# Kernel optimization log

Hardware: AMD Instinct MI355X
Metric: run time of the kernel (lower is better)

The kernel has to match this reference:

```python
import jax, jax.numpy as jnp
import numpy as np

N_NODES = 100000
N_EDGES = 1200000
NODE_DIM = 128
HIDDEN = 64
N_POSTS = 50000


def setup_inputs() -> dict:
    key = jax.random.key(0)
    ks = jax.random.split(key, 10)
    s = 1.0 / np.sqrt(NODE_DIM)
    sh = 1.0 / np.sqrt(HIDDEN)
    return {
        "node_features": jax.random.normal(ks[0], (N_NODES, NODE_DIM), dtype=jnp.float32),
        "edge_index": jax.random.randint(ks[1], (2, N_EDGES), 0, N_NODES, dtype=jnp.int64) if jax.config.jax_enable_x64 else jax.random.randint(ks[1], (2, N_EDGES), 0, N_NODES, dtype=jnp.int32),
        "post_mask": jax.random.randint(ks[2], (N_POSTS,), 0, N_NODES, dtype=jnp.int32),
        "W_enc": jax.random.uniform(ks[3], (NODE_DIM, HIDDEN), jnp.float32, -s, s),
        "b_enc": jax.random.uniform(ks[4], (HIDDEN,), jnp.float32, -s, s),
        "W_conv": jax.random.uniform(ks[5], (HIDDEN, HIDDEN), jnp.float32, -sh, sh),
        "b_conv": jax.random.uniform(ks[6], (HIDDEN,), jnp.float32, -sh, sh),
        "W_out": jax.random.uniform(ks[7], (HIDDEN, 1), jnp.float32, -sh, sh),
        "b_out": jax.random.uniform(ks[8], (1,), jnp.float32, -sh, sh),
    }


def reference(node_features, edge_index, post_mask, W_enc, b_enc, W_conv, b_conv, W_out, b_out):
    # encode: relu(Linear)
    node_emb = jax.nn.relu(node_features @ W_enc + b_enc)  # [N, H]
    src, dst = edge_index[0], edge_index[1]
    # per-edge gather then scatter-add into destination nodes (segment sum)
    messages = jax.ops.segment_sum(node_emb[src], dst, num_segments=node_emb.shape[0])  # [N, H]
    node_emb = jax.nn.relu((node_emb + messages) @ W_conv + b_conv)  # [N, H]
    post_emb = node_emb[post_mask]  # [P, H]
    out = jax.nn.sigmoid((post_emb @ W_out + b_out).squeeze(-1))  # [P]
    return out
```

## Files before the change

kernel.cpp:

```cpp
#include <hip/hip_runtime.h>
#include <hip/hip_bf16.h>
#include <math.h>


#define HIDDEN 64
#define NODE_DIM 128
#define SCAN_CHUNK 1024

typedef __attribute__((ext_vector_type(8))) short short8;
typedef __attribute__((ext_vector_type(4))) float floatx4;

union F2B { short8 s; __hip_bfloat162 h[4]; };

__device__ inline short8 cvt8(const float4& p, const float4& q) {
    F2B u;
    u.h[0] = __float22bfloat162_rn(make_float2(p.x, p.y));
    u.h[1] = __float22bfloat162_rn(make_float2(p.z, p.w));
    u.h[2] = __float22bfloat162_rn(make_float2(q.x, q.y));
    u.h[3] = __float22bfloat162_rn(make_float2(q.z, q.w));
    return u.s;
}

__device__ inline void cvt8_split(const float4& p, const float4& q,
                                  short8& hi, short8& lo) {
    const float f[8] = {p.x, p.y, p.z, p.w, q.x, q.y, q.z, q.w};
    F2B uh, ul;
    #pragma unroll
    for (int jj = 0; jj < 4; ++jj) {
        const float2 v = make_float2(f[2 * jj], f[2 * jj + 1]);
        const __hip_bfloat162 h = __float22bfloat162_rn(v);
        const float2 hv = __bfloat1622float2(h);
        ul.h[jj] = __float22bfloat162_rn(make_float2(v.x - hv.x, v.y - hv.y));
        uh.h[jj] = h;
    }
    hi = uh.s; lo = ul.s;
}

__global__ __launch_bounds__(256) void k_encode_mfma(
    const float* __restrict__ A, const float* __restrict__ We,
    const float* __restrict__ be, __hip_bfloat16* __restrict__ emb16, int n_tiles)
{
    const int lane = threadIdx.x & 63;
    const int r    = lane & 15;
    const int quad = lane >> 4;

    short8 Wb[4][4];
    #pragma unroll
    for (int ks = 0; ks < 4; ++ks) {
        #pragma unroll
        for (int nt = 0; nt < 4; ++nt) {
            F2B u;
            #pragma unroll
            for (int jj = 0; jj < 4; ++jj) {
                const int k0 = ks * 32 + quad * 8 + 2 * jj;
                const float lo = We[(size_t)k0 * HIDDEN + nt * 16 + r];
                const float hi = We[(size_t)(k0 + 1) * HIDDEN + nt * 16 + r];
                u.h[jj] = __float22bfloat162_rn(make_float2(lo, hi));
            }
            Wb[ks][nt] = u.s;
        }
    }
    float bias[4];
    #pragma unroll
    for (int nt = 0; nt < 4; ++nt) bias[nt] = be[nt * 16 + r];

    const int wid    = (blockIdx.x * 256 + threadIdx.x) >> 6;
    const int nwaves = gridDim.x * 4;
    for (int t = wid; t < n_tiles; t += nwaves) {
        const float* Arow = A + (size_t)t * 16 * NODE_DIM + (size_t)r * NODE_DIM + quad * 8;
        float4 a[4][2];
        #pragma unroll
        for (int ks = 0; ks < 4; ++ks) {
            a[ks][0] = *(const float4*)(Arow + ks * 32);
            a[ks][1] = *(const float4*)(Arow + ks * 32 + 4);
        }
        floatx4 acc[4] = {};
        #pragma unroll
        for (int ks = 0; ks < 4; ++ks) {
            const short8 af = cvt8(a[ks][0], a[ks][1]);
            #pragma unroll
            for (int nt = 0; nt < 4; ++nt)
                acc[nt] = __builtin_amdgcn_mfma_f32_16x16x32_bf16(af, Wb[ks][nt], acc[nt], 0, 0, 0);
        }
        #pragma unroll
        for (int nt = 0; nt < 4; ++nt) {
            #pragma unroll
            for (int g = 0; g < 4; ++g) {
                const int node = t * 16 + quad * 4 + g;
                const float h = fmaxf(acc[nt][g] + bias[nt], 0.0f);
                emb16[(size_t)node * HIDDEN + nt * 16 + r] = __float2bfloat16(h);
            }
        }
    }
}

__global__ __launch_bounds__(64) void k_encode_tail(
    const float* __restrict__ A, const float* __restrict__ We,
    const float* __restrict__ be, __hip_bfloat16* __restrict__ emb16, int base)
{
    const int lane = threadIdx.x;
    const int n = base + blockIdx.x;
    const float* row = A + (size_t)n * NODE_DIM;
    float acc = be[lane];
    for (int k = 0; k < NODE_DIM; ++k)
        acc = fmaf(row[k], We[(size_t)k * HIDDEN + lane], acc);
    emb16[(size_t)n * HIDDEN + lane] = __float2bfloat16(fmaxf(acc, 0.0f));
}

__global__ __launch_bounds__(256) void k_setflags(
    const int* __restrict__ post, int* __restrict__ flag,
    unsigned int* __restrict__ bits,
    int* __restrict__ nodelist, int* __restrict__ inv,
    int* __restrict__ listCnt, int n_posts)
{
    const int p = blockIdx.x * 256 + threadIdx.x;
    if (p >= n_posts) return;
    const int n = post[p];
    atomicOr(&bits[n >> 5], 1u << (n & 31));
    if (atomicCAS(&flag[n], 0, 1) == 0) {
        const int i = atomicAdd(listCnt, 1);
        nodelist[i] = n;
        inv[n] = i;
    }
}

__global__ __launch_bounds__(256) void k_count(
    const int* __restrict__ dsts, const unsigned int* __restrict__ bits,
    int* __restrict__ count, int n_edges)
{
    const int stride = gridDim.x * 256;
    for (int e = blockIdx.x * 256 + threadIdx.x; e < n_edges; e += stride) {
        const int d = dsts[e];
        if ((bits[d >> 5] >> (d & 31)) & 1u) atomicAdd(&count[d], 1);
    }
}

__global__ __launch_bounds__(256) void k_scan_lb(
    const int* __restrict__ count, int* __restrict__ row_start,
    unsigned int* __restrict__ partials, int n)
{
    __shared__ int s[256];
    __shared__ int sExc;
    const int b = blockIdx.x, tid = threadIdx.x;
    const int base = b * SCAN_CHUNK + tid * 4;
    int c0 = (base + 0 < n) ? count[base + 0] : 0;
    int c1 = (base + 1 < n) ? count[base + 1] : 0;
    int c2 = (base + 2 < n) ? count[base + 2] : 0;
    int c3 = (base + 3 < n) ? count[base + 3] : 0;
    const int t = c0 + c1 + c2 + c3;
    s[tid] = t;
    __syncthreads();
    #pragma unroll
    for (int off = 1; off < 256; off <<= 1) {
        int v = (tid >= off) ? s[tid - off] : 0;
        __syncthreads();
        s[tid] += v;
        __syncthreads();
    }
    if (tid == 0) {
        const unsigned int total = (unsigned int)s[255];
        if (b == 0) {
            __hip_atomic_store(&partials[0], (2u << 30) | total,
                               __ATOMIC_RELEASE, __HIP_MEMORY_SCOPE_AGENT);
            sExc = 0;
        } else {
            __hip_atomic_store(&partials[b], (1u << 30) | total,
                               __ATOMIC_RELEASE, __HIP_MEMORY_SCOPE_AGENT);
            int exc = 0;
            int j = b - 1;
            while (true) {
                const unsigned int v = __hip_atomic_load(&partials[j],
                    __ATOMIC_ACQUIRE, __HIP_MEMORY_SCOPE_AGENT);
                const unsigned int st = v >> 30;
                if (st == 0u) continue;
                exc += (int)(v & 0x3FFFFFFFu);
                if (st == 2u) break;
                --j;
            }
            __hip_atomic_store(&partials[b], (2u << 30) | (unsigned int)(exc + (int)total),
                               __ATOMIC_RELEASE, __HIP_MEMORY_SCOPE_AGENT);
            sExc = exc;
        }
    }
    __syncthreads();
    int run = sExc + s[tid] - t;
    if (base + 0 < n) row_start[base + 0] = run;           run += c0;
    if (base + 1 < n) row_start[base + 1] = run;           run += c1;
    if (base + 2 < n) row_start[base + 2] = run;           run += c2;
    if (base + 3 < n) row_start[base + 3] = run;
}

__global__ __launch_bounds__(256) void k_fill(
    const int* __restrict__ srcs, const int* __restrict__ dsts,
    const unsigned int* __restrict__ bits, int* __restrict__ row_start,
    int* __restrict__ slots, int n_edges)
{
    const int stride = gridDim.x * 256;
    for (int e = blockIdx.x * 256 + threadIdx.x; e < n_edges; e += stride) {
        const int d = dsts[e];
        if (!((bits[d >> 5] >> (d & 31)) & 1u)) continue;
        const int idx = atomicAdd(&row_start[d], 1);
        slots[idx] = srcs[e];
    }
}

__global__ __launch_bounds__(256) void k_gather(
    const int* __restrict__ nodelist, const int* __restrict__ listCnt,
    const int* __restrict__ row_end, const int* __restrict__ count,
    const int* __restrict__ slots, const __hip_bfloat16* __restrict__ emb16,
    float* __restrict__ msg_c)
{
    const int lane = threadIdx.x & 63;
    const int j    = lane & 7;
    const int g    = lane >> 3;
    const int gw   = (blockIdx.x * 256 + threadIdx.x) >> 6;
    const int nw   = gridDim.x * 4;
    const int nc   = listCnt[0];

    for (int i = gw; i < nc; i += nw) {
        const int n    = nodelist[i];
        const int m    = count[n];
        const int base = row_end[n] - m;

        float2 a0 = {0.f, 0.f}, a1 = {0.f, 0.f}, a2 = {0.f, 0.f}, a3 = {0.f, 0.f};
        #define ACC8(v)  do { F2B u; u.s = (v); float2 t;                       \
            t = __bfloat1622float2(u.h[0]); a0.x += t.x; a0.y += t.y;           \
            t = __bfloat1622float2(u.h[1]); a1.x += t.x; a1.y += t.y;           \
            t = __bfloat1622float2(u.h[2]); a2.x += t.x; a2.y += t.y;           \
            t = __bfloat1622float2(u.h[3]); a3.x += t.x; a3.y += t.y; } while (0)

        if (g == 0) {
            const short8 v = *(const short8*)(emb16 + (size_t)n * HIDDEN + j * 8);
            ACC8(v);
        }
        int c = g;
        for (; c + 8 < m; c += 16) {
            const int s0 = slots[base + c];
            const int s1 = slots[base + c + 8];
            const short8 v0 = *(const short8*)(emb16 + (size_t)s0 * HIDDEN + j * 8);
            const short8 v1 = *(const short8*)(emb16 + (size_t)s1 * HIDDEN + j * 8);
            ACC8(v0); ACC8(v1);
        }
        for (; c < m; c += 8) {
            const int s0 = slots[base + c];
            const short8 v0 = *(const short8*)(emb16 + (size_t)s0 * HIDDEN + j * 8);
            ACC8(v0);
        }
        #undef ACC8

        #pragma unroll
        for (int off = 8; off < 64; off <<= 1) {
            a0.x += __shfl_xor(a0.x, off); a0.y += __shfl_xor(a0.y, off);
            a1.x += __shfl_xor(a1.x, off); a1.y += __shfl_xor(a1.y, off);
            a2.x += __shfl_xor(a2.x, off); a2.y += __shfl_xor(a2.y, off);
            a3.x += __shfl_xor(a3.x, off); a3.y += __shfl_xor(a3.y, off);
        }
        if (g == 0) {
            float4* dst = (float4*)(msg_c + (size_t)i * HIDDEN + j * 8);
            dst[0] = make_float4(a0.x, a0.y, a1.x, a1.y);
            dst[1] = make_float4(a2.x, a2.y, a3.x, a3.y);
        }
    }
}

__global__ __launch_bounds__(256) void k_head_mfma(
    const int* __restrict__ listCnt, const float* __restrict__ msg_c,
    const float* __restrict__ Wc, const float* __restrict__ bc,
    const float* __restrict__ Wo, const float* __restrict__ bo,
    float* __restrict__ res_c)
{
    const int lane = threadIdx.x & 63;
    const int r    = lane & 15;
    const int quad = lane >> 4;

    short8 Wb[2][4];
    #pragma unroll
    for (int ks = 0; ks < 2; ++ks) {
        #pragma unroll
        for (int nt = 0; nt < 4; ++nt) {
            F2B u;
            #pragma unroll
            for (int jj = 0; jj < 4; ++jj) {
                const int k0 = ks * 32 + quad * 8 + 2 * jj;
                const float lo = Wc[(size_t)k0 * HIDDEN + nt * 16 + r];
                const float hi = Wc[(size_t)(k0 + 1) * HIDDEN + nt * 16 + r];
                u.h[jj] = __float22bfloat162_rn(make_float2(lo, hi));
            }
            Wb[ks][nt] = u.s;
        }
    }
    float bias[4], wo[4];
    #pragma unroll
    for (int nt = 0; nt < 4; ++nt) { bias[nt] = bc[nt * 16 + r]; wo[nt] = Wo[nt * 16 + r]; }
    const float bo_s = bo[0];

    const int nc      = listCnt[0];
    const int n_tiles = (nc + 15) / 16;
    const int wid     = (blockIdx.x * 256 + threadIdx.x) >> 6;
    const int nwaves  = gridDim.x * 4;

    for (int tile = wid; tile < n_tiles; tile += nwaves) {
        const int i0  = tile * 16;
        const int row = i0 + r;
        floatx4 acc[4] = {};
        #pragma unroll
        for (int ks = 0; ks < 2; ++ks) {
            float4 f0 = make_float4(0.f, 0.f, 0.f, 0.f), f1 = f0;
            if (row < nc) {
                const float* src = msg_c + (size_t)row * HIDDEN + ks * 32 + quad * 8;
                f0 = *(const float4*)src;
                f1 = *(const float4*)(src + 4);
            }
            short8 ah, al;
            cvt8_split(f0, f1, ah, al);
            #pragma unroll
            for (int nt = 0; nt < 4; ++nt) {
                acc[nt] = __builtin_amdgcn_mfma_f32_16x16x32_bf16(ah, Wb[ks][nt], acc[nt], 0, 0, 0);
                acc[nt] = __builtin_amdgcn_mfma_f32_16x16x32_bf16(al, Wb[ks][nt], acc[nt], 0, 0, 0);
            }
        }
        float res[4];
        #pragma unroll
        for (int gg = 0; gg < 4; ++gg) {
            float part = 0.0f;
            #pragma unroll
            for (int nt = 0; nt < 4; ++nt)
                part += fmaxf(acc[nt][gg] + bias[nt], 0.0f) * wo[nt];
            part += __shfl_xor(part, 1);
            part += __shfl_xor(part, 2);
            part += __shfl_xor(part, 4);
            part += __shfl_xor(part, 8);
            res[gg] = part;
        }
        if (r == 0) {
            #pragma unroll
            for (int gg = 0; gg < 4; ++gg) {
                const int idx = i0 + quad * 4 + gg;
                if (idx < nc)
                    res_c[idx] = 1.0f / (1.0f + __expf(-(res[gg] + bo_s)));
            }
        }
    }
}

__global__ __launch_bounds__(256) void k_out(
    const int* __restrict__ post, const int* __restrict__ inv,
    const float* __restrict__ res_c, float* __restrict__ out, int n_posts)
{
    const int p = blockIdx.x * 256 + threadIdx.x;
    if (p < n_posts) out[p] = res_c[inv[post[p]]];
}

extern "C" void kernel_launch(void* const* d_in, const int* in_sizes, int n_in,
                              void* d_out, int out_size, void* d_ws, size_t ws_size,
                              hipStream_t stream) {
    const float* A    = (const float*)d_in[0];
    const int*   ei   = (const int*)  d_in[1];
    const int*   post = (const int*)  d_in[2];
    const float* We   = (const float*)d_in[3];
    const float* be   = (const float*)d_in[4];
    const float* Wc   = (const float*)d_in[5];
    const float* bc   = (const float*)d_in[6];
    const float* Wo   = (const float*)d_in[7];
    const float* bo   = (const float*)d_in[8];
    float* out = (float*)d_out;

    const int n_nodes = in_sizes[0] / NODE_DIM;
    const int n_edges = in_sizes[1] / 2;
    const int n_posts = in_sizes[2];

    char* p = (char*)d_ws;
    __hip_bfloat16* emb16 = (__hip_bfloat16*)p;  p += (size_t)n_nodes * HIDDEN * 2;
    float* msg_c    = (float*)p;              p += (size_t)n_posts * HIDDEN * 4;
    int*   slots    = (int*)p;                p += (size_t)n_edges * 4;
    int*   flag     = (int*)p;                p += (size_t)n_nodes * 4;
    int*   count    = (int*)p;                p += (size_t)n_nodes * 4;
    int*   listCnt  = (int*)p;                p += 256;
    unsigned int* partials = (unsigned int*)p; p += 512;
    unsigned int* bits = (unsigned int*)p;    p += 16384;
    int*   row_start= (int*)p;                p += (size_t)n_nodes * 4;
    int*   nodelist = (int*)p;                p += (size_t)n_nodes * 4;
    int*   inv      = (int*)p;                p += (size_t)n_nodes * 4;
    float* res_c    = (float*)p;              p += (size_t)n_posts * 4;

    const int* srcs = ei;
    const int* dsts = ei + n_edges;
    const int nb = (n_nodes + SCAN_CHUNK - 1) / SCAN_CHUNK;
    const int n_tiles = n_nodes / 16;
    const int rem     = n_nodes - n_tiles * 16;

    hipMemsetAsync(flag, 0, (size_t)n_nodes * 8 + 256 + 512 + 16384, stream);
    k_setflags<<<(n_posts + 255) / 256, 256, 0, stream>>>(post, flag, bits, nodelist, inv, listCnt, n_posts);
    k_encode_mfma<<<(n_tiles + 3) / 4, 256, 0, stream>>>(A, We, be, emb16, n_tiles);
    if (rem > 0)
        k_encode_tail<<<rem, 64, 0, stream>>>(A, We, be, emb16, n_tiles * 16);
    k_count<<<2048, 256, 0, stream>>>(dsts, bits, count, n_edges);
    k_scan_lb<<<nb, 256, 0, stream>>>(count, row_start, partials, n_nodes);
    k_fill<<<2048, 256, 0, stream>>>(srcs, dsts, bits, row_start, slots, n_edges);
    k_gather<<<8192, 256, 0, stream>>>(nodelist, listCnt, row_start, count, slots, emb16, msg_c);
    k_head_mfma<<<1024, 256, 0, stream>>>(listCnt, msg_c, Wc, bc, Wo, bo, res_c);
    k_out<<<(n_posts + 255) / 256, 256, 0, stream>>>(post, inv, res_c, out, n_posts);
}
```

Measured before the change: 223.4 us.

## Fuse encode and CSR build into one persistent kernel with grid barriers

Merges encode, setflags, count, scan and fill into a single persistent kernel. Blocks are split into an encode group and a CSR-build group that run at the same time, and the build phases are separated by software grid barriers on atomic counters. The aim is to cut five launches and their serial gaps and to overlap the encode matmul with the edge counting and filling. This depends on every build block being co-resident for the spin barriers. The encode now runs on fewer blocks, the scan needs at least 98 build blocks, and the flag array is replaced by the bitset's atomicOr return value.

```diff
diff --git a/kernel.cpp b/kernel.cpp
--- a/kernel.cpp
+++ b/kernel.cpp
@@ -36,171 +36,176 @@
     hi = uh.s; lo = ul.s;
 }
 
-__global__ __launch_bounds__(256) void k_encode_mfma(
-    const float* __restrict__ A, const float* __restrict__ We,
-    const float* __restrict__ be, __hip_bfloat16* __restrict__ emb16, int n_tiles)
+__device__ inline void cbar(int* ctr, int target) {
+    __syncthreads();
+    if (threadIdx.x == 0) {
+        __builtin_amdgcn_fence(__ATOMIC_RELEASE, "agent");
+        __hip_atomic_fetch_add(ctr, 1, __ATOMIC_RELAXED, __HIP_MEMORY_SCOPE_AGENT);
+        while (__hip_atomic_load(ctr, __ATOMIC_RELAXED, __HIP_MEMORY_SCOPE_AGENT) < target)
+            __builtin_amdgcn_s_sleep(8);
+        __builtin_amdgcn_fence(__ATOMIC_ACQUIRE, "agent");
+    }
+    __syncthreads();
+}
+
+struct BuildP {
+    const float* A; const int* srcs; const int* dsts; const int* post;
+    const float* We; const float* be;
+    __hip_bfloat16* emb16;
+    int* slots; int* count; int* listCnt;
+    unsigned int* partials; unsigned int* bits;
+    int* row_start; int* nodelist; int* inv; int* bars;
+    int n_nodes, n_edges, n_posts, n_tiles, eblk, cblk;
+};
+
+__global__ __launch_bounds__(256, 2) void k_build(BuildP P)
 {
-    const int lane = threadIdx.x & 63;
+    const int tid  = threadIdx.x;
+    const int lane = tid & 63;
     const int r    = lane & 15;
     const int quad = lane >> 4;
 
-    short8 Wb[4][4];
-    #pragma unroll
-    for (int ks = 0; ks < 4; ++ks) {
-        #pragma unroll
-        for (int nt = 0; nt < 4; ++nt) {
-            F2B u;
-            #pragma unroll
-            for (int jj = 0; jj < 4; ++jj) {
-                const int k0 = ks * 32 + quad * 8 + 2 * jj;
-                const float lo = We[(size_t)k0 * HIDDEN + nt * 16 + r];
-                const float hi = We[(size_t)(k0 + 1) * HIDDEN + nt * 16 + r];
-                u.h[jj] = __float22bfloat162_rn(make_float2(lo, hi));
-            }
-            Wb[ks][nt] = u.s;
-        }
-    }
-    float bias[4];
-    #pragma unroll
-    for (int nt = 0; nt < 4; ++nt) bias[nt] = be[nt * 16 + r];
-
-    const int wid    = (blockIdx.x * 256 + threadIdx.x) >> 6;
-    const int nwaves = gridDim.x * 4;
-    for (int t = wid; t < n_tiles; t += nwaves) {
-        const float* Arow = A + (size_t)t * 16 * NODE_DIM + (size_t)r * NODE_DIM + quad * 8;
-        float4 a[4][2];
-        #pragma unroll
-        for (int ks = 0; ks < 4; ++ks) {
-            a[ks][0] = *(const float4*)(Arow + ks * 32);
-            a[ks][1] = *(const float4*)(Arow + ks * 32 + 4);
-        }
-        floatx4 acc[4] = {};
-        #pragma unroll
-        for (int ks = 0; ks < 4; ++ks) {
-            const short8 af = cvt8(a[ks][0], a[ks][1]);
+    if ((int)blockIdx.x < P.eblk) {
+        short8 Wb[4][4];
+        #pragma unroll
+        for (int ks = 0; ks < 4; ++ks)
+            #pragma unroll
+            for (int nt = 0; nt < 4; ++nt) {
+                F2B u;
+                #pragma unroll
+                for (int jj = 0; jj < 4; ++jj) {
+                    const int k0 = ks * 32 + quad * 8 + 2 * jj;
+                    const float lo = P.We[(size_t)k0 * HIDDEN + nt * 16 + r];
+                    const float hi = P.We[(size_t)(k0 + 1) * HIDDEN + nt * 16 + r];
+                    u.h[jj] = __float22bfloat162_rn(make_float2(lo, hi));
+                }
+                Wb[ks][nt] = u.s;
+            }
+        float bias[4];
+        #pragma unroll
+        for (int nt = 0; nt < 4; ++nt) bias[nt] = P.be[nt * 16 + r];
+
+        const int widE = blockIdx.x * 4 + (tid >> 6);
+        const int nwE  = P.eblk * 4;
+        for (int t = widE; t < P.n_tiles; t += nwE) {
+            const float* Arow = P.A + (size_t)t * 16 * NODE_DIM + (size_t)r * NODE_DIM + quad * 8;
+            float4 a[4][2];
+            #pragma unroll
+            for (int ks = 0; ks < 4; ++ks) {
+                a[ks][0] = *(const float4*)(Arow + ks * 32);
+                a[ks][1] = *(const float4*)(Arow + ks * 32 + 4);
+            }
+            floatx4 acc[4] = {};
+            #pragma unroll
+            for (int ks = 0; ks < 4; ++ks) {
+                const short8 af = cvt8(a[ks][0], a[ks][1]);
+                #pragma unroll
+                for (int nt = 0; nt < 4; ++nt)
+                    acc[nt] = __builtin_amdgcn_mfma_f32_16x16x32_bf16(af, Wb[ks][nt], acc[nt], 0, 0, 0);
+            }
             #pragma unroll
             for (int nt = 0; nt < 4; ++nt)
-                acc[nt] = __builtin_amdgcn_mfma_f32_16x16x32_bf16(af, Wb[ks][nt], acc[nt], 0, 0, 0);
-        }
-        #pragma unroll
-        for (int nt = 0; nt < 4; ++nt) {
-            #pragma unroll
-            for (int g = 0; g < 4; ++g) {
-                const int node = t * 16 + quad * 4 + g;
-                const float h = fmaxf(acc[nt][g] + bias[nt], 0.0f);
-                emb16[(size_t)node * HIDDEN + nt * 16 + r] = __float2bfloat16(h);
-            }
-        }
-    }
-}
-
-__global__ __launch_bounds__(64) void k_encode_tail(
-    const float* __restrict__ A, const float* __restrict__ We,
-    const float* __restrict__ be, __hip_bfloat16* __restrict__ emb16, int base)
-{
-    const int lane = threadIdx.x;
-    const int n = base + blockIdx.x;
-    const float* row = A + (size_t)n * NODE_DIM;
-    float acc = be[lane];
-    for (int k = 0; k < NODE_DIM; ++k)
-        acc = fmaf(row[k], We[(size_t)k * HIDDEN + lane], acc);
-    emb16[(size_t)n * HIDDEN + lane] = __float2bfloat16(fmaxf(acc, 0.0f));
-}
-
-__global__ __launch_bounds__(256) void k_setflags(
-    const int* __restrict__ post, int* __restrict__ flag,
-    unsigned int* __restrict__ bits,
-    int* __restrict__ nodelist, int* __restrict__ inv,
-    int* __restrict__ listCnt, int n_posts)
-{
-    const int p = blockIdx.x * 256 + threadIdx.x;
-    if (p >= n_posts) return;
-    const int n = post[p];
-    atomicOr(&bits[n >> 5], 1u << (n & 31));
-    if (atomicCAS(&flag[n], 0, 1) == 0) {
-        const int i = atomicAdd(listCnt, 1);
-        nodelist[i] = n;
-        inv[n] = i;
-    }
-}
-
-__global__ __launch_bounds__(256) void k_count(
-    const int* __restrict__ dsts, const unsigned int* __restrict__ bits,
-    int* __restrict__ count, int n_edges)
-{
-    const int stride = gridDim.x * 256;
-    for (int e = blockIdx.x * 256 + threadIdx.x; e < n_edges; e += stride) {
-        const int d = dsts[e];
-        if ((bits[d >> 5] >> (d & 31)) & 1u) atomicAdd(&count[d], 1);
-    }
-}
-
-__global__ __launch_bounds__(256) void k_scan_lb(
-    const int* __restrict__ count, int* __restrict__ row_start,
-    unsigned int* __restrict__ partials, int n)
-{
-    __shared__ int s[256];
-    __shared__ int sExc;
-    const int b = blockIdx.x, tid = threadIdx.x;
-    const int base = b * SCAN_CHUNK + tid * 4;
-    int c0 = (base + 0 < n) ? count[base + 0] : 0;
-    int c1 = (base + 1 < n) ? count[base + 1] : 0;
-    int c2 = (base + 2 < n) ? count[base + 2] : 0;
-    int c3 = (base + 3 < n) ? count[base + 3] : 0;
-    const int t = c0 + c1 + c2 + c3;
-    s[tid] = t;
-    __syncthreads();
-    #pragma unroll
-    for (int off = 1; off < 256; off <<= 1) {
-        int v = (tid >= off) ? s[tid - off] : 0;
-        __syncthreads();
-        s[tid] += v;
-        __syncthreads();
-    }
-    if (tid == 0) {
-        const unsigned int total = (unsigned int)s[255];
-        if (b == 0) {
-            __hip_atomic_store(&partials[0], (2u << 30) | total,
-                               __ATOMIC_RELEASE, __HIP_MEMORY_SCOPE_AGENT);
-            sExc = 0;
-        } else {
-            __hip_atomic_store(&partials[b], (1u << 30) | total,
-                               __ATOMIC_RELEASE, __HIP_MEMORY_SCOPE_AGENT);
-            int exc = 0;
-            int j = b - 1;
-            while (true) {
-                const unsigned int v = __hip_atomic_load(&partials[j],
-                    __ATOMIC_ACQUIRE, __HIP_MEMORY_SCOPE_AGENT);
-                const unsigned int st = v >> 30;
-                if (st == 0u) continue;
-                exc += (int)(v & 0x3FFFFFFFu);
-                if (st == 2u) break;
-                --j;
-            }
-            __hip_atomic_store(&partials[b], (2u << 30) | (unsigned int)(exc + (int)total),
-                               __ATOMIC_RELEASE, __HIP_MEMORY_SCOPE_AGENT);
-            sExc = exc;
-        }
-    }
-    __syncthreads();
-    int run = sExc + s[tid] - t;
-    if (base + 0 < n) row_start[base + 0] = run;           run += c0;
-    if (base + 1 < n) row_start[base + 1] = run;           run += c1;
-    if (base + 2 < n) row_start[base + 2] = run;           run += c2;
-    if (base + 3 < n) row_start[base + 3] = run;
-}
-
-__global__ __launch_bounds__(256) void k_fill(
-    const int* __restrict__ srcs, const int* __restrict__ dsts,
-    const unsigned int* __restrict__ bits, int* __restrict__ row_start,
-    int* __restrict__ slots, int n_edges)
-{
-    const int stride = gridDim.x * 256;
-    for (int e = blockIdx.x * 256 + threadIdx.x; e < n_edges; e += stride) {
-        const int d = dsts[e];
-        if (!((bits[d >> 5] >> (d & 31)) & 1u)) continue;
-        const int idx = atomicAdd(&row_start[d], 1);
-        slots[idx] = srcs[e];
+                #pragma unroll
+                for (int g = 0; g < 4; ++g) {
+                    const int node = t * 16 + quad * 4 + g;
+                    const float h = fmaxf(acc[nt][g] + bias[nt], 0.0f);
+                    P.emb16[(size_t)node * HIDDEN + nt * 16 + r] = __float2bfloat16(h);
+                }
+        }
+        const int rem = P.n_nodes - P.n_tiles * 16;
+        if (rem > 0 && widE == 0) {
+            for (int n = P.n_tiles * 16; n < P.n_nodes; ++n) {
+                float acc = P.be[lane];
+                const float* row = P.A + (size_t)n * NODE_DIM;
+                for (int k = 0; k < NODE_DIM; ++k)
+                    acc = fmaf(row[k], P.We[(size_t)k * HIDDEN + lane], acc);
+                P.emb16[(size_t)n * HIDDEN + lane] = __float2bfloat16(fmaxf(acc, 0.0f));
+            }
+        }
+    } else {
+        const int cb    = blockIdx.x - P.eblk;
+        const int ctid  = cb * 256 + tid;
+        const int cstep = P.cblk * 256;
+
+        for (int p = ctid; p < P.n_posts; p += cstep) {
+            const int n = P.post[p];
+            const unsigned int bit = 1u << (n & 31);
+            const unsigned int old = atomicOr(&P.bits[n >> 5], bit);
+            if (!(old & bit)) {
+                const int i = atomicAdd(P.listCnt, 1);
+                P.nodelist[i] = n;
+                P.inv[n] = i;
+            }
+        }
+        cbar(P.bars + 0, P.cblk);
+
+        for (int e = ctid; e < P.n_edges; e += cstep) {
+            const int d = P.dsts[e];
+            if ((P.bits[d >> 5] >> (d & 31)) & 1u) atomicAdd(&P.count[d], 1);
+        }
+        cbar(P.bars + 1, P.cblk);
+
+        {
+            __shared__ int s[256];
+            __shared__ int sExc;
+            const int nb = (P.n_nodes + SCAN_CHUNK - 1) / SCAN_CHUNK;
+            if (cb < nb) {
+                const int base = cb * SCAN_CHUNK + tid * 4;
+                const int n = P.n_nodes;
+                int c0 = (base + 0 < n) ? P.count[base + 0] : 0;
+                int c1 = (base + 1 < n) ? P.count[base + 1] : 0;
+                int c2 = (base + 2 < n) ? P.count[base + 2] : 0;
+                int c3 = (base + 3 < n) ? P.count[base + 3] : 0;
+                const int t4 = c0 + c1 + c2 + c3;
+                s[tid] = t4;
+                __syncthreads();
+                #pragma unroll
+                for (int off = 1; off < 256; off <<= 1) {
+                    int v = (tid >= off) ? s[tid - off] : 0;
+                    __syncthreads();
+                    s[tid] += v;
+                    __syncthreads();
+                }
+                if (tid == 0) {
+                    const unsigned int total = (unsigned int)s[255];
+                    if (cb == 0) {
+                        __hip_atomic_store(&P.partials[0], (2u << 30) | total,
+                                           __ATOMIC_RELEASE, __HIP_MEMORY_SCOPE_AGENT);
+                        sExc = 0;
+                    } else {
+                        __hip_atomic_store(&P.partials[cb], (1u << 30) | total,
+                                           __ATOMIC_RELEASE, __HIP_MEMORY_SCOPE_AGENT);
+                        int exc = 0, j = cb - 1;
+                        while (true) {
+                            const unsigned int v = __hip_atomic_load(&P.partials[j],
+                                __ATOMIC_ACQUIRE, __HIP_MEMORY_SCOPE_AGENT);
+                            const unsigned int st = v >> 30;
+                            if (st == 0u) { __builtin_amdgcn_s_sleep(1); continue; }
+                            exc += (int)(v & 0x3FFFFFFFu);
+                            if (st == 2u) break;
+                            --j;
+                        }
+                        __hip_atomic_store(&P.partials[cb], (2u << 30) | (unsigned int)(exc + (int)total),
+                                           __ATOMIC_RELEASE, __HIP_MEMORY_SCOPE_AGENT);
+                        sExc = exc;
+                    }
+                }
+                __syncthreads();
+                int run = sExc + s[tid] - t4;
+                if (base + 0 < n) P.row_start[base + 0] = run;   run += c0;
+                if (base + 1 < n) P.row_start[base + 1] = run;   run += c1;
+                if (base + 2 < n) P.row_start[base + 2] = run;   run += c2;
+                if (base + 3 < n) P.row_start[base + 3] = run;
+            }
+        }
+        cbar(P.bars + 2, P.cblk);
+
+        for (int e = ctid; e < P.n_edges; e += cstep) {
+            const int d = P.dsts[e];
+            if (!((P.bits[d >> 5] >> (d & 31)) & 1u)) continue;
+            const int idx = atomicAdd(&P.row_start[d], 1);
+            P.slots[idx] = P.srcs[e];
+        }
     }
 }
 
@@ -275,7 +280,7 @@
 
     short8 Wb[2][4];
     #pragma unroll
-    for (int ks = 0; ks < 2; ++ks) {
+    for (int ks = 0; ks < 2; ++ks)
         #pragma unroll
         for (int nt = 0; nt < 4; ++nt) {
             F2B u;
@@ -288,7 +293,6 @@
             }
             Wb[ks][nt] = u.s;
         }
-    }
     float bias[4], wo[4];
     #pragma unroll
     for (int nt = 0; nt < 4; ++nt) { bias[nt] = bc[nt * 16 + r]; wo[nt] = Wo[nt * 16 + r]; }
@@ -354,50 +358,58 @@
 extern "C" void kernel_launch(void* const* d_in, const int* in_sizes, int n_in,
                               void* d_out, int out_size, void* d_ws, size_t ws_size,
                               hipStream_t stream) {
-    const float* A    = (const float*)d_in[0];
-    const int*   ei   = (const int*)  d_in[1];
-    const int*   post = (const int*)  d_in[2];
-    const float* We   = (const float*)d_in[3];
-    const float* be   = (const float*)d_in[4];
-    const float* Wc   = (const float*)d_in[5];
-    const float* bc   = (const float*)d_in[6];
-    const float* Wo   = (const float*)d_in[7];
-    const float* bo   = (const float*)d_in[8];
+    BuildP P;
+    P.A    = (const float*)d_in[0];
+    const int* ei = (const int*)d_in[1];
+    P.post = (const int*)d_in[2];
+    P.We   = (const float*)d_in[3];
+    P.be   = (const float*)d_in[4];
+    const float* Wc = (const float*)d_in[5];
+    const float* bc = (const float*)d_in[6];
+    const float* Wo = (const float*)d_in[7];
+    const float* bo = (const float*)d_in[8];
     float* out = (float*)d_out;
 
-    const int n_nodes = in_sizes[0] / NODE_DIM;
-    const int n_edges = in_sizes[1] / 2;
-    const int n_posts = in_sizes[2];
+    P.n_nodes = in_sizes[0] / NODE_DIM;
+    P.n_edges = in_sizes[1] / 2;
+    P.n_posts = in_sizes[2];
+    P.n_tiles = P.n_nodes / 16;
+    P.srcs = ei;
+    P.dsts = ei + P.n_edges;
 
     char* p = (char*)d_ws;
-    __hip_bfloat16* emb16 = (__hip_bfloat16*)p;  p += (size_t)n_nodes * HIDDEN * 2;
-    float* msg_c    = (float*)p;              p += (size_t)n_posts * HIDDEN * 4;
-    int*   slots    = (int*)p;                p += (size_t)n_edges * 4;
-    int*   flag     = (int*)p;                p += (size_t)n_nodes * 4;
-    int*   count    = (int*)p;                p += (size_t)n_nodes * 4;
-    int*   listCnt  = (int*)p;                p += 256;
-    unsigned int* partials = (unsigned int*)p; p += 512;
-    unsigned int* bits = (unsigned int*)p;    p += 16384;
-    int*   row_start= (int*)p;                p += (size_t)n_nodes * 4;
-    int*   nodelist = (int*)p;                p += (size_t)n_nodes * 4;
-    int*   inv      = (int*)p;                p += (size_t)n_nodes * 4;
-    float* res_c    = (float*)p;              p += (size_t)n_posts * 4;
-
-    const int* srcs = ei;
-    const int* dsts = ei + n_edges;
-    const int nb = (n_nodes + SCAN_CHUNK - 1) / SCAN_CHUNK;
-    const int n_tiles = n_nodes / 16;
-    const int rem     = n_nodes - n_tiles * 16;
-
-    hipMemsetAsync(flag, 0, (size_t)n_nodes * 8 + 256 + 512 + 16384, stream);
-    k_setflags<<<(n_posts + 255) / 256, 256, 0, stream>>>(post, flag, bits, nodelist, inv, listCnt, n_posts);
-    k_encode_mfma<<<(n_tiles + 3) / 4, 256, 0, stream>>>(A, We, be, emb16, n_tiles);
-    if (rem > 0)
-        k_encode_tail<<<rem, 64, 0, stream>>>(A, We, be, emb16, n_tiles * 16);
-    k_count<<<2048, 256, 0, stream>>>(dsts, bits, count, n_edges);
-    k_scan_lb<<<nb, 256, 0, stream>>>(count, row_start, partials, n_nodes);
-    k_fill<<<2048, 256, 0, stream>>>(srcs, dsts, bits, row_start, slots, n_edges);
-    k_gather<<<8192, 256, 0, stream>>>(nodelist, listCnt, row_start, count, slots, emb16, msg_c);
-    k_head_mfma<<<1024, 256, 0, stream>>>(listCnt, msg_c, Wc, bc, Wo, bo, res_c);
-    k_out<<<(n_posts + 255) / 256, 256, 0, stream>>>(post, inv, res_c, out, n_posts);
-}
+    P.emb16 = (__hip_bfloat16*)p;   p += (size_t)P.n_nodes * HIDDEN * 2;
+    float* msg_c = (float*)p;       p += (size_t)P.n_posts * HIDDEN * 4;
+    P.slots = (int*)p;              p += (size_t)P.n_edges * 4;
+    char* zbase = p;
+    P.count    = (int*)p;           p += (size_t)P.n_nodes * 4;
+    P.bits     = (unsigned int*)p;  p += ((size_t)(P.n_nodes + 31) / 32 + 32) * 4;
+    P.listCnt  = (int*)p;           p += 256;
+    P.partials = (unsigned int*)p;  p += 1024;
+    P.bars     = (int*)p;           p += 256;
+    const size_t zbytes = (size_t)(p - zbase);
+    P.row_start = (int*)p;          p += (size_t)P.n_nodes * 4;
+    P.nodelist  = (int*)p;          p += (size_t)P.n_nodes * 4;
+    P.inv       = (int*)p;          p += (size_t)P.n_nodes * 4;
+    float* res_c = (float*)p;       p += (size_t)P.n_posts * 4;
+
+    int ncu = 256;
+    hipDeviceGetAttribute(&ncu, hipDeviceAttributeMultiprocessorCount, 0);
+    int occ = 0;
+    if (hipOccupancyMaxActiveBlocksPerMultiprocessor(&occ, k_build, 256, 0) != hipSuccess || occ < 1)
+        occ = 1;
+    int grid = occ * ncu;
+    if (grid > 512) grid = 512;
+    int cblk = (grid * 3) / 8;
+    if (cblk < 98) cblk = 98;
+    if (cblk > grid - 4) cblk = grid - 4;
+    P.cblk = cblk;
+    P.eblk = grid - cblk;
+
+    hipMemsetAsync(zbase, 0, zbytes, stream);
+    k_build<<<grid, 256, 0, stream>>>(P);
+    k_gather<<<8192, 256, 0, stream>>>(P.nodelist, P.listCnt, P.row_start, P.count,
+                                       P.slots, P.emb16, msg_c);
+    k_head_mfma<<<1024, 256, 0, stream>>>(P.listCnt, msg_c, Wc, bc, Wo, bo, res_c);
+    k_out<<<(P.n_posts + 255) / 256, 256, 0, stream>>>(P.post, P.inv, res_c, out, P.n_posts);
+}
```

Measured after the change: 241.9 us. +8.3%, slower.
